# Optimization experiments

Hardware: AMD Instinct MI355X
Metric: run time of the kernel (lower is better)

Reference implementation:

```python
import jax, jax.numpy as jnp
import numpy as np

H = 1024  # lstm_hidden_dim

def setup_inputs() -> dict:
    key = jax.random.key(0)
    ks = jax.random.split(key, 8)
    T, E, V = 2048, 512, 32000
    return {
        "sentence": jax.random.randint(ks[0], (1, T), 0, V, dtype=jnp.int32),
        "emb": jax.random.normal(ks[1], (V, E), dtype=jnp.float32) * 0.1,
        "Wi": jax.random.normal(ks[2], (E, 4 * H), dtype=jnp.float32) * (1.0 / np.sqrt(H)),
        "Wh": jax.random.normal(ks[3], (H, 4 * H), dtype=jnp.float32) * (1.0 / np.sqrt(H)),
        "bi": jax.random.normal(ks[4], (4 * H,), dtype=jnp.float32) * 0.01,
        "bh": jax.random.normal(ks[5], (4 * H,), dtype=jnp.float32) * 0.01,
        "fc_w": jax.random.normal(ks[6], (V, H), dtype=jnp.float32) * (1.0 / np.sqrt(H)),
        "fc_b": jnp.zeros((V,), dtype=jnp.float32),
    }

def _lstm(x, Wi, Wh, bi, bh):
    # x: (T, E). Batch is 1 in the original (input viewed as (1, -1, E)).
    # Precompute input contribution for all timesteps (hoists the big GEMM out of the loop).
    xg = x @ Wi + bi + bh  # (T, 4H)

    def step(carry, g):
        h, c = carry  # (H,), (H,)
        gates = g + h @ Wh  # (4H,)
        i_g, f_g, c_g, o_g = jnp.split(gates, 4)
        i_g = jax.nn.sigmoid(i_g)
        f_g = jax.nn.sigmoid(f_g)
        c_g = jnp.tanh(c_g)
        o_g = jax.nn.sigmoid(o_g)
        c = f_g * c + i_g * c_g
        h = o_g * jnp.tanh(c)
        return (h, c), h

    init = (jnp.zeros((Wh.shape[0],), x.dtype), jnp.zeros((Wh.shape[0],), x.dtype))
    _, hs = jax.lax.scan(step, init, xg)  # hs: (T, H)
    return hs

def reference(sentence, emb, Wi, Wh, bi, bh, fc_w, fc_b):
    x = emb[sentence.reshape(-1)]  # (T, E)
    hs = _lstm(x, Wi, Wh, bi, bh)  # (T, H)
    logits = jax.nn.relu(hs @ fc_w.T + fc_b)  # (T, V)
    return jax.nn.log_softmax(logits, axis=1)  # is_test=False path
```

## Files before the change

### kernel.cpp

```cpp
#include <hip/hip_runtime.h>
#include <hip/hip_bf16.h>
#include <cmath>

#define T_LEN 2048
#define E_DIM 512
#define H_DIM 1024
#define G_DIM 4096
#define V_DIM 32000
#define LSTM_NB 256

typedef unsigned short ushortx8 __attribute__((ext_vector_type(8)));
typedef unsigned short ushortx4 __attribute__((ext_vector_type(4)));
typedef short shortx8 __attribute__((ext_vector_type(8)));
typedef float floatx4 __attribute__((ext_vector_type(4)));
typedef unsigned uintx4 __attribute__((ext_vector_type(4)));

__device__ __forceinline__ float bf2f(unsigned short u) {
    return __uint_as_float(((unsigned)u) << 16);
}
__device__ __forceinline__ unsigned short f2bf(float f) {
    __hip_bfloat16 b = __float2bfloat16(f);
    return *reinterpret_cast<unsigned short*>(&b);
}
__device__ __forceinline__ float fast_sigmoid(float x) {
    return 1.f / (1.f + __expf(-x));
}
__device__ __forceinline__ float fast_tanh(float x) {
    return 1.f - 2.f / (__expf(2.f * x) + 1.f);
}

__global__ __launch_bounds__(256) void prep_kernel(const float* __restrict__ Wh,
                                                   unsigned short* __restrict__ whTp)
{
    const int c0  = blockIdx.x * 16;
    const int tid = threadIdx.x;
    const int cc  = tid & 15;
    const int kk  = tid >> 4;
    const int col = c0 + cc;
    unsigned short* dst = whTp + (size_t)col * H_DIM;
    #pragma unroll 4
    for (int r = 0; r < 64; ++r) {
        const int i = r * 16 + kk;
        float v = Wh[(size_t)i * G_DIM + col];
        const int pos = ((i & 255) >> 2) * 16 + (i >> 8) * 4 + (i & 3);
        dst[pos] = f2bf(v);
    }
}

__global__ __launch_bounds__(256) void embconv_kernel(const float* __restrict__ src,
                                                      unsigned short* __restrict__ dst)
{
    const size_t i = ((size_t)blockIdx.x * 256 + threadIdx.x) * 8;
    float4 a = *reinterpret_cast<const float4*>(src + i);
    float4 b = *reinterpret_cast<const float4*>(src + i + 4);
    ushortx8 o;
    o[0] = f2bf(a.x); o[1] = f2bf(a.y); o[2] = f2bf(a.z); o[3] = f2bf(a.w);
    o[4] = f2bf(b.x); o[5] = f2bf(b.y); o[6] = f2bf(b.z); o[7] = f2bf(b.w);
    *reinterpret_cast<ushortx8*>(dst + i) = o;
}

__global__ __launch_bounds__(256) void wiconv_kernel(const float* __restrict__ Wi,
                                                     unsigned short* __restrict__ wiT)
{
    __shared__ float tile[32][33];
    const int nb = blockIdx.x * 32;
    const int kb = blockIdx.y * 32;
    const int tx = threadIdx.x & 31;
    const int ty = threadIdx.x >> 5;
    #pragma unroll
    for (int i = 0; i < 32; i += 8)
        tile[ty + i][tx] = Wi[(size_t)(kb + ty + i) * G_DIM + nb + tx];
    __syncthreads();
    #pragma unroll
    for (int i = 0; i < 32; i += 8)
        wiT[(size_t)(nb + ty + i) * E_DIM + kb + tx] = f2bf(tile[tx][ty + i]);
}

__global__ __launch_bounds__(256) void fcwconv_kernel(const float* __restrict__ src,
                                                      unsigned short* __restrict__ dst)
{
    const size_t i = ((size_t)blockIdx.x * 256 + threadIdx.x) * 8;
    float4 a = *reinterpret_cast<const float4*>(src + i);
    float4 b = *reinterpret_cast<const float4*>(src + i + 4);
    ushortx8 o;
    o[0] = f2bf(a.x); o[1] = f2bf(a.y); o[2] = f2bf(a.z); o[3] = f2bf(a.w);
    o[4] = f2bf(b.x); o[5] = f2bf(b.y); o[6] = f2bf(b.z); o[7] = f2bf(b.w);
    *reinterpret_cast<ushortx8*>(dst + i) = o;
}

__global__ __launch_bounds__(256) void xg_mfma_kernel(const int* __restrict__ sent,
                                                      const unsigned short* __restrict__ embb,
                                                      const unsigned short* __restrict__ wiT,
                                                      const float* __restrict__ bi,
                                                      const float* __restrict__ bh,
                                                      unsigned short* __restrict__ xg)
{
    const int tid  = threadIdx.x;
    const int w    = tid >> 6;
    const int lane = tid & 63;
    const int n0 = blockIdx.x * 64;
    const int m0 = blockIdx.y * 128;
    const int lrow = lane & 15;
    const int lk   = (lane >> 4) * 8;

    const int r0 = sent[m0 + w * 32 + lrow];
    const int r1 = sent[m0 + w * 32 + 16 + lrow];

    floatx4 acc[2][4] = {};
    const unsigned short* a0p = embb + (size_t)r0 * E_DIM + lk;
    const unsigned short* a1p = embb + (size_t)r1 * E_DIM + lk;
    const unsigned short* b0p = wiT + (size_t)(n0 + lrow) * E_DIM + lk;

    for (int k0 = 0; k0 < E_DIM; k0 += 32) {
        shortx8 a0 = *reinterpret_cast<const shortx8*>(a0p + k0);
        shortx8 a1 = *reinterpret_cast<const shortx8*>(a1p + k0);
        shortx8 b0 = *reinterpret_cast<const shortx8*>(b0p + k0);
        shortx8 b1 = *reinterpret_cast<const shortx8*>(b0p + 16 * E_DIM + k0);
        shortx8 b2 = *reinterpret_cast<const shortx8*>(b0p + 32 * E_DIM + k0);
        shortx8 b3 = *reinterpret_cast<const shortx8*>(b0p + 48 * E_DIM + k0);
        acc[0][0] = __builtin_amdgcn_mfma_f32_16x16x32_bf16(a0, b0, acc[0][0], 0, 0, 0);
        acc[0][1] = __builtin_amdgcn_mfma_f32_16x16x32_bf16(a0, b1, acc[0][1], 0, 0, 0);
        acc[0][2] = __builtin_amdgcn_mfma_f32_16x16x32_bf16(a0, b2, acc[0][2], 0, 0, 0);
        acc[0][3] = __builtin_amdgcn_mfma_f32_16x16x32_bf16(a0, b3, acc[0][3], 0, 0, 0);
        acc[1][0] = __builtin_amdgcn_mfma_f32_16x16x32_bf16(a1, b0, acc[1][0], 0, 0, 0);
        acc[1][1] = __builtin_amdgcn_mfma_f32_16x16x32_bf16(a1, b1, acc[1][1], 0, 0, 0);
        acc[1][2] = __builtin_amdgcn_mfma_f32_16x16x32_bf16(a1, b2, acc[1][2], 0, 0, 0);
        acc[1][3] = __builtin_amdgcn_mfma_f32_16x16x32_bf16(a1, b3, acc[1][3], 0, 0, 0);
    }

    #pragma unroll
    for (int j = 0; j < 4; ++j) {
        const int c = n0 + j * 16 + lrow;
        const float bias = bi[c] + bh[c];
        #pragma unroll
        for (int i = 0; i < 2; ++i) {
            #pragma unroll
            for (int reg = 0; reg < 4; ++reg) {
                const int r = m0 + w * 32 + i * 16 + (lane >> 4) * 4 + reg;
                xg[(size_t)r * G_DIM + c] = f2bf(acc[i][j][reg] + bias);
            }
        }
    }
}

__global__ __launch_bounds__(256) void lstm_kernel(const unsigned short* __restrict__ xg,
                                                   const unsigned short* __restrict__ whTp,
                                                   unsigned* __restrict__ hbuf,
                                                   int T)
{
    const int b    = blockIdx.x;
    const int tid  = threadIdx.x;
    const int w    = tid >> 6;
    const int lane = tid & 63;
    const int s    = b * 4;

    __shared__ float h_lds[H_DIM];

    float c_val = 0.0f;

    for (int t = 0; t < T; ++t) {
        float xr[4] = {0.f, 0.f, 0.f, 0.f};
        if (lane == 0) {
            #pragma unroll
            for (int q = 0; q < 4; ++q)
                xr[q] = bf2f(xg[(size_t)t * G_DIM + (q << 10) + s + w]);
        }

        if (t) {
            const unsigned* pp = hbuf + (size_t)(t - 1) * H_DIM + tid * 4;
            const unsigned tg = (unsigned)t;
            uintx4 v;
            int guard = 0;
            bool ok;
            do {
                asm volatile("global_load_dwordx4 %0, %1, off sc0 sc1\n\t"
                             "s_waitcnt vmcnt(0)"
                             : "=&v"(v) : "v"(pp) : "memory");
                ok = ((v[0] >> 16) == tg) & ((v[1] >> 16) == tg)
                   & ((v[2] >> 16) == tg) & ((v[3] >> 16) == tg);
            } while (!ok && ++guard < 8192);
            floatx4 hv;
            hv[0] = __uint_as_float(v[0] << 16);
            hv[1] = __uint_as_float(v[1] << 16);
            hv[2] = __uint_as_float(v[2] << 16);
            hv[3] = __uint_as_float(v[3] << 16);
            *reinterpret_cast<floatx4*>(&h_lds[tid * 4]) = hv;
        } else {
            floatx4 z = {0.f, 0.f, 0.f, 0.f};
            *reinterpret_cast<floatx4*>(&h_lds[tid * 4]) = z;
        }
        __syncthreads();

        float hreg[16];
        #pragma unroll
        for (int c = 0; c < 4; ++c) {
            floatx4 hv = *reinterpret_cast<const floatx4*>(&h_lds[c * 256 + lane * 4]);
            hreg[c * 4 + 0] = hv[0]; hreg[c * 4 + 1] = hv[1];
            hreg[c * 4 + 2] = hv[2]; hreg[c * 4 + 3] = hv[3];
        }

        float sums[4];
        #pragma unroll
        for (int q = 0; q < 4; ++q) {
            const ushortx8* wp = reinterpret_cast<const ushortx8*>(
                whTp + ((size_t)((q << 10) + s + w)) * H_DIM + lane * 16);
            ushortx8 w0 = wp[0];
            ushortx8 w1 = wp[1];
            float sm = 0.f;
            #pragma unroll
            for (int e = 0; e < 8; ++e) sm += bf2f(w0[e]) * hreg[e];
            #pragma unroll
            for (int e = 0; e < 8; ++e) sm += bf2f(w1[e]) * hreg[8 + e];
            #pragma unroll
            for (int off = 32; off; off >>= 1) sm += __shfl_xor(sm, off, 64);
            sums[q] = sm;
        }

        if (lane == 0) {
            float ig = fast_sigmoid(sums[0] + xr[0]);
            float fg = fast_sigmoid(sums[1] + xr[1]);
            float gg = fast_tanh(sums[2] + xr[2]);
            float og = fast_sigmoid(sums[3] + xr[3]);
            c_val = fg * c_val + ig * gg;
            float h = og * fast_tanh(c_val);
            unsigned pk = ((unsigned)(t + 1) << 16) | (unsigned)f2bf(h);
            unsigned* sp = hbuf + (size_t)t * H_DIM + s + w;
            asm volatile("global_store_dword %0, %1, off sc0 sc1"
                         :: "v"(sp), "v"(pk) : "memory");
        }
    }
}

__global__ __launch_bounds__(256) void hconv_kernel(const unsigned* __restrict__ hbuf,
                                                    unsigned short* __restrict__ hb)
{
    const size_t i = ((size_t)blockIdx.x * 256 + threadIdx.x) * 4;
    uintx4 v = *reinterpret_cast<const uintx4*>(hbuf + i);
    ushortx4 o;
    #pragma unroll
    for (int q = 0; q < 4; ++q)
        o[q] = (unsigned short)(v[q] & 0xFFFFu);
    *reinterpret_cast<ushortx4*>(hb + i) = o;
}

__global__ __launch_bounds__(256) void fc_kernel(const unsigned short* __restrict__ hb,
                                                 const unsigned short* __restrict__ fcwb,
                                                 const float* __restrict__ fcb,
                                                 float* __restrict__ out)
{
    const int tid  = threadIdx.x;
    const int w    = tid >> 6;
    const int lane = tid & 63;
    const int n0 = blockIdx.x * 64;
    const int m0 = blockIdx.y * 128;
    const int lrow = lane & 15;
    const int lk   = (lane >> 4) * 8;

    floatx4 acc[2][4] = {};
    const unsigned short* a0p = hb + (size_t)(m0 + w * 32 + lrow) * H_DIM + lk;
    const unsigned short* a1p = a0p + 16 * H_DIM;
    const unsigned short* b0p = fcwb + (size_t)(n0 + lrow) * H_DIM + lk;

    for (int k0 = 0; k0 < H_DIM; k0 += 32) {
        shortx8 a0 = *reinterpret_cast<const shortx8*>(a0p + k0);
        shortx8 a1 = *reinterpret_cast<const shortx8*>(a1p + k0);
        shortx8 b0 = *reinterpret_cast<const shortx8*>(b0p + k0);
        shortx8 b1 = *reinterpret_cast<const shortx8*>(b0p + 16 * H_DIM + k0);
        shortx8 b2 = *reinterpret_cast<const shortx8*>(b0p + 32 * H_DIM + k0);
        shortx8 b3 = *reinterpret_cast<const shortx8*>(b0p + 48 * H_DIM + k0);
        acc[0][0] = __builtin_amdgcn_mfma_f32_16x16x32_bf16(a0, b0, acc[0][0], 0, 0, 0);
        acc[0][1] = __builtin_amdgcn_mfma_f32_16x16x32_bf16(a0, b1, acc[0][1], 0, 0, 0);
        acc[0][2] = __builtin_amdgcn_mfma_f32_16x16x32_bf16(a0, b2, acc[0][2], 0, 0, 0);
        acc[0][3] = __builtin_amdgcn_mfma_f32_16x16x32_bf16(a0, b3, acc[0][3], 0, 0, 0);
        acc[1][0] = __builtin_amdgcn_mfma_f32_16x16x32_bf16(a1, b0, acc[1][0], 0, 0, 0);
        acc[1][1] = __builtin_amdgcn_mfma_f32_16x16x32_bf16(a1, b1, acc[1][1], 0, 0, 0);
        acc[1][2] = __builtin_amdgcn_mfma_f32_16x16x32_bf16(a1, b2, acc[1][2], 0, 0, 0);
        acc[1][3] = __builtin_amdgcn_mfma_f32_16x16x32_bf16(a1, b3, acc[1][3], 0, 0, 0);
    }

    #pragma unroll
    for (int j = 0; j < 4; ++j) {
        const int c = n0 + j * 16 + lrow;
        const float bias = fcb[c];
        #pragma unroll
        for (int i = 0; i < 2; ++i) {
            #pragma unroll
            for (int reg = 0; reg < 4; ++reg) {
                const int r = m0 + w * 32 + i * 16 + (lane >> 4) * 4 + reg;
                out[(size_t)r * V_DIM + c] = fmaxf(acc[i][j][reg] + bias, 0.f);
            }
        }
    }
}

__global__ __launch_bounds__(256) void lsm_kernel(float* __restrict__ out)
{
    const int row = blockIdx.x;
    float* p = out + (size_t)row * V_DIM;
    const int tid = threadIdx.x;
    __shared__ float ms[256], ss[256];

    float m = -1e30f, sacc = 0.f;
    for (int i4 = tid; i4 < V_DIM / 4; i4 += 256) {
        float4 v = *reinterpret_cast<const float4*>(p + i4 * 4);
        float vm = fmaxf(fmaxf(v.x, v.y), fmaxf(v.z, v.w));
        if (vm > m) { sacc *= __expf(m - vm); m = vm; }
        sacc += __expf(v.x - m) + __expf(v.y - m) + __expf(v.z - m) + __expf(v.w - m);
    }
    ms[tid] = m; ss[tid] = sacc; __syncthreads();
    for (int sft = 128; sft; sft >>= 1) {
        if (tid < sft) {
            float m2 = ms[tid + sft], s2 = ss[tid + sft];
            float mm = fmaxf(ms[tid], m2);
            ss[tid] = ss[tid] * __expf(ms[tid] - mm) + s2 * __expf(m2 - mm);
            ms[tid] = mm;
        }
        __syncthreads();
    }
    const float L = ms[0] + logf(ss[0]);

    for (int i4 = tid; i4 < V_DIM / 4; i4 += 256) {
        float4 v = *reinterpret_cast<const float4*>(p + i4 * 4);
        v.x -= L; v.y -= L; v.z -= L; v.w -= L;
        *reinterpret_cast<float4*>(p + i4 * 4) = v;
    }
}

extern "C" void kernel_launch(void* const* d_in, const int* in_sizes, int n_in,
                              void* d_out, int out_size, void* d_ws, size_t ws_size,
                              hipStream_t stream)
{
    const int*   sent = (const int*)  d_in[0];
    const float* emb  = (const float*)d_in[1];
    const float* Wi   = (const float*)d_in[2];
    const float* Wh   = (const float*)d_in[3];
    const float* bi   = (const float*)d_in[4];
    const float* bh   = (const float*)d_in[5];
    const float* fcw  = (const float*)d_in[6];
    const float* fcb  = (const float*)d_in[7];
    float* out = (float*)d_out;

    uint8_t* ws = (uint8_t*)d_ws;
    size_t off = 0;
    unsigned*       hbuf = (unsigned*)(ws + off);       off += (size_t)T_LEN * H_DIM * 4;
    unsigned short* xg   = (unsigned short*)(ws + off); off += (size_t)T_LEN * G_DIM * 2;
    unsigned short* whTp = (unsigned short*)(ws + off); off += (size_t)G_DIM * H_DIM * 2;
    unsigned short* hb   = (unsigned short*)(ws + off); off += (size_t)T_LEN * H_DIM * 2;
    uint8_t* R = ws + off;
    unsigned short* fcwb = (unsigned short*)R;
    unsigned short* embb = (unsigned short*)R;
    unsigned short* wiT  = (unsigned short*)(R + (size_t)V_DIM * E_DIM * 2);

    hipMemsetAsync(hbuf, 0, (size_t)T_LEN * H_DIM * 4, stream);
    embconv_kernel<<<(int)(((size_t)V_DIM * E_DIM / 8) / 256), 256, 0, stream>>>(emb, embb);
    wiconv_kernel<<<dim3(G_DIM / 32, E_DIM / 32), 256, 0, stream>>>(Wi, wiT);
    prep_kernel<<<G_DIM / 16, 256, 0, stream>>>(Wh, whTp);
    xg_mfma_kernel<<<dim3(G_DIM / 64, T_LEN / 128), 256, 0, stream>>>(sent, embb, wiT, bi, bh, xg);
    fcwconv_kernel<<<(int)(((size_t)V_DIM * H_DIM / 8) / 256), 256, 0, stream>>>(fcw, fcwb);
    lstm_kernel<<<LSTM_NB, 256, 0, stream>>>(xg, whTp, hbuf, T_LEN);
    hconv_kernel<<<(int)(((size_t)T_LEN * H_DIM / 4) / 256), 256, 0, stream>>>(hbuf, hb);
    fc_kernel<<<dim3(V_DIM / 64, T_LEN / 128), 256, 0, stream>>>(hb, fcwb, fcb, out);
    lsm_kernel<<<T_LEN, 256, 0, stream>>>(out);
}
```

Before: 5.795 ms.

## Replicate LSTM hidden-state exchange into ring buffers and interleave gate inputs

The recurrent h exchange between blocks moves from a full T×H tagged buffer to a small 4-deep ring that is replicated 8 times. Each block polls the replica chosen by its block index, which spreads the polling load across more memory lines. The xg layout is interleaved per hidden unit so one 8-byte load fetches all four gate inputs, and the LSTM writes bf16 h directly, which removes the separate conversion kernel. The cost is 8 coherent stores per output per step instead of one. The 4-deep ring relies on the step tags to stop a slow block from reading an overwritten slot.

Result: faster. 5.525 ms (-4.7%).

```diff
diff --git a/kernel.cpp b/kernel.cpp
--- a/kernel.cpp
+++ b/kernel.cpp
@@ -8,6 +8,8 @@
 #define G_DIM 4096
 #define V_DIM 32000
 #define LSTM_NB 256
+#define NREP 8
+#define RING 4
 
 typedef unsigned short ushortx8 __attribute__((ext_vector_type(8)));
 typedef unsigned short ushortx4 __attribute__((ext_vector_type(4)));
@@ -93,7 +95,7 @@
                                                       const unsigned short* __restrict__ wiT,
                                                       const float* __restrict__ bi,
                                                       const float* __restrict__ bh,
-                                                      unsigned short* __restrict__ xg)
+                                                      unsigned short* __restrict__ xg2)
 {
     const int tid  = threadIdx.x;
     const int w    = tid >> 6;
@@ -131,21 +133,24 @@
     #pragma unroll
     for (int j = 0; j < 4; ++j) {
         const int c = n0 + j * 16 + lrow;
+        const int hidx = c & 1023;
+        const int gate = c >> 10;
         const float bias = bi[c] + bh[c];
         #pragma unroll
         for (int i = 0; i < 2; ++i) {
             #pragma unroll
             for (int reg = 0; reg < 4; ++reg) {
                 const int r = m0 + w * 32 + i * 16 + (lane >> 4) * 4 + reg;
-                xg[(size_t)r * G_DIM + c] = f2bf(acc[i][j][reg] + bias);
+                xg2[(size_t)r * G_DIM + hidx * 4 + gate] = f2bf(acc[i][j][reg] + bias);
             }
         }
     }
 }
 
-__global__ __launch_bounds__(256) void lstm_kernel(const unsigned short* __restrict__ xg,
+__global__ __launch_bounds__(256) void lstm_kernel(const unsigned short* __restrict__ xg2,
                                                    const unsigned short* __restrict__ whTp,
-                                                   unsigned* __restrict__ hbuf,
+                                                   unsigned* __restrict__ ring,
+                                                   unsigned short* __restrict__ hb,
                                                    int T)
 {
     const int b    = blockIdx.x;
@@ -153,6 +158,7 @@
     const int w    = tid >> 6;
     const int lane = tid & 63;
     const int s    = b * 4;
+    const int rep  = b & (NREP - 1);
 
     __shared__ float h_lds[H_DIM];
 
@@ -161,13 +167,15 @@
     for (int t = 0; t < T; ++t) {
         float xr[4] = {0.f, 0.f, 0.f, 0.f};
         if (lane == 0) {
-            #pragma unroll
-            for (int q = 0; q < 4; ++q)
-                xr[q] = bf2f(xg[(size_t)t * G_DIM + (q << 10) + s + w]);
+            ushortx4 xv = *reinterpret_cast<const ushortx4*>(
+                xg2 + (size_t)t * G_DIM + (size_t)(s + w) * 4);
+            #pragma unroll
+            for (int q = 0; q < 4; ++q) xr[q] = bf2f(xv[q]);
         }
 
         if (t) {
-            const unsigned* pp = hbuf + (size_t)(t - 1) * H_DIM + tid * 4;
+            const unsigned* pp = ring + ((t - 1) & (RING - 1)) * (NREP * H_DIM)
+                                      + rep * H_DIM + tid * 4;
             const unsigned tg = (unsigned)t;
             uintx4 v;
             int guard = 0;
@@ -223,24 +231,18 @@
             float og = fast_sigmoid(sums[3] + xr[3]);
             c_val = fg * c_val + ig * gg;
             float h = og * fast_tanh(c_val);
-            unsigned pk = ((unsigned)(t + 1) << 16) | (unsigned)f2bf(h);
-            unsigned* sp = hbuf + (size_t)t * H_DIM + s + w;
-            asm volatile("global_store_dword %0, %1, off sc0 sc1"
-                         :: "v"(sp), "v"(pk) : "memory");
-        }
-    }
-}
-
-__global__ __launch_bounds__(256) void hconv_kernel(const unsigned* __restrict__ hbuf,
-                                                    unsigned short* __restrict__ hb)
-{
-    const size_t i = ((size_t)blockIdx.x * 256 + threadIdx.x) * 4;
-    uintx4 v = *reinterpret_cast<const uintx4*>(hbuf + i);
-    ushortx4 o;
-    #pragma unroll
-    for (int q = 0; q < 4; ++q)
-        o[q] = (unsigned short)(v[q] & 0xFFFFu);
-    *reinterpret_cast<ushortx4*>(hb + i) = o;
+            const unsigned short hbf = f2bf(h);
+            const unsigned pk = ((unsigned)(t + 1) << 16) | (unsigned)hbf;
+            unsigned* base = ring + (t & (RING - 1)) * (NREP * H_DIM) + s + w;
+            #pragma unroll
+            for (int r = 0; r < NREP; ++r) {
+                unsigned* sp = base + r * H_DIM;
+                asm volatile("global_store_dword %0, %1, off sc0 sc1"
+                             :: "v"(sp), "v"(pk) : "memory");
+            }
+            hb[(size_t)t * H_DIM + s + w] = hbf;
+        }
+    }
 }
 
 __global__ __launch_bounds__(256) void fc_kernel(const unsigned short* __restrict__ hb,
@@ -342,8 +344,8 @@
 
     uint8_t* ws = (uint8_t*)d_ws;
     size_t off = 0;
-    unsigned*       hbuf = (unsigned*)(ws + off);       off += (size_t)T_LEN * H_DIM * 4;
-    unsigned short* xg   = (unsigned short*)(ws + off); off += (size_t)T_LEN * G_DIM * 2;
+    unsigned*       ring = (unsigned*)(ws + off);       off += (size_t)RING * NREP * H_DIM * 4;
+    unsigned short* xg2  = (unsigned short*)(ws + off); off += (size_t)T_LEN * G_DIM * 2;
     unsigned short* whTp = (unsigned short*)(ws + off); off += (size_t)G_DIM * H_DIM * 2;
     unsigned short* hb   = (unsigned short*)(ws + off); off += (size_t)T_LEN * H_DIM * 2;
     uint8_t* R = ws + off;
@@ -351,14 +353,13 @@
     unsigned short* embb = (unsigned short*)R;
     unsigned short* wiT  = (unsigned short*)(R + (size_t)V_DIM * E_DIM * 2);
 
-    hipMemsetAsync(hbuf, 0, (size_t)T_LEN * H_DIM * 4, stream);
+    hipMemsetAsync(ring, 0, (size_t)RING * NREP * H_DIM * 4, stream);
     embconv_kernel<<<(int)(((size_t)V_DIM * E_DIM / 8) / 256), 256, 0, stream>>>(emb, embb);
     wiconv_kernel<<<dim3(G_DIM / 32, E_DIM / 32), 256, 0, stream>>>(Wi, wiT);
     prep_kernel<<<G_DIM / 16, 256, 0, stream>>>(Wh, whTp);
-    xg_mfma_kernel<<<dim3(G_DIM / 64, T_LEN / 128), 256, 0, stream>>>(sent, embb, wiT, bi, bh, xg);
+    xg_mfma_kernel<<<dim3(G_DIM / 64, T_LEN / 128), 256, 0, stream>>>(sent, embb, wiT, bi, bh, xg2);
     fcwconv_kernel<<<(int)(((size_t)V_DIM * H_DIM / 8) / 256), 256, 0, stream>>>(fcw, fcwb);
-    lstm_kernel<<<LSTM_NB, 256, 0, stream>>>(xg, whTp, hbuf, T_LEN);
-    hconv_kernel<<<(int)(((size_t)T_LEN * H_DIM / 4) / 256), 256, 0, stream>>>(hbuf, hb);
+    lstm_kernel<<<LSTM_NB, 256, 0, stream>>>(xg2, whTp, ring, hb, T_LEN);
     fc_kernel<<<dim3(V_DIM / 64, T_LEN / 128), 256, 0, stream>>>(hb, fcwb, fcb, out);
     lsm_kernel<<<T_LEN, 256, 0, stream>>>(out);
 }
```
